# Kernel optimization log

Hardware: AMD Instinct MI355X
Metric: run time of the kernel (lower is better)

Reference implementation:

```python
import jax, jax.numpy as jnp
import numpy as np

NUM_NODES = 100_000
NUM_EDGES = 1_200_000
NUM_REL = 3
EMBED_DIM = 64
HIDDEN_DIM = 64
NUM_CLS = 2
NUM_GRAPHS = 512


def setup_inputs() -> dict:
    key = jax.random.key(0)
    ks = jax.random.split(key, 12)
    s = 1.0 / np.sqrt(EMBED_DIM)
    inp = {
        # forward args
        "x": jnp.zeros((NUM_NODES,), dtype=jnp.int64),  # vocab size 1 -> all zeros
        "edge_index": jax.random.randint(ks[0], (2, NUM_EDGES), 0, NUM_NODES, dtype=jnp.int64),
        "edge_type": jax.random.randint(ks[1], (NUM_EDGES,), 0, NUM_REL, dtype=jnp.int64),
        "batch": jnp.sort(jax.random.randint(ks[2], (NUM_NODES,), 0, NUM_GRAPHS, dtype=jnp.int64)),
        # parameters
        "embed_w": jax.random.normal(ks[3], (1, EMBED_DIM), jnp.float32),
        "W1": jax.random.normal(ks[4], (NUM_REL, EMBED_DIM, HIDDEN_DIM), jnp.float32) * s,
        "root1": jax.random.normal(ks[5], (EMBED_DIM, HIDDEN_DIM), jnp.float32) * s,
        "b1": jnp.zeros((HIDDEN_DIM,), jnp.float32),
        "W2": jax.random.normal(ks[6], (NUM_REL, HIDDEN_DIM, HIDDEN_DIM), jnp.float32) * s,
        "root2": jax.random.normal(ks[7], (HIDDEN_DIM, HIDDEN_DIM), jnp.float32) * s,
        "b2": jnp.zeros((HIDDEN_DIM,), jnp.float32),
        "lin_w": jax.random.normal(ks[8], (HIDDEN_DIM, NUM_CLS), jnp.float32) * s,
        "lin_b": jnp.zeros((NUM_CLS,), jnp.float32),
    }
    return inp


def rgcn_conv(h, W, root, b, src, dst, edge_type):
    """PyG RGCNConv with mean aggregation per relation + root weight + bias."""
    n = h.shape[0]
    out = h @ root + b  # root/self contribution, [N, H]
    for r in range(NUM_REL):
        m = (edge_type == r).astype(h.dtype)  # [E]
        tr = h @ W[r]                          # [N, H] small GEMM
        msg = tr[src] * m[:, None]             # gather [E, H]
        ssum = jax.ops.segment_sum(msg, dst, num_segments=n)  # scatter-add [N, H]
        cnt = jax.ops.segment_sum(m, dst, num_segments=n)     # per-relation in-degree
        out = out + ssum / jnp.clip(cnt, 1.0)[:, None]        # mean aggregation
    return out


def reference(x, edge_index, edge_type, batch, embed_w, W1, root1, b1, W2, root2, b2, lin_w, lin_b):
    src, dst = edge_index[0], edge_index[1]
    h = embed_w[x]                                       # [N, D] embedding lookup
    h = jax.nn.relu(rgcn_conv(h, W1, root1, b1, src, dst, edge_type))
    h = jax.nn.relu(rgcn_conv(h, W2, root2, b2, src, dst, edge_type))
    # global mean pool over graphs
    gsum = jax.ops.segment_sum(h, batch, num_segments=NUM_GRAPHS)            # [G, H]
    gcnt = jax.ops.segment_sum(jnp.ones_like(h[:, 0]), batch, num_segments=NUM_GRAPHS)
    g_emb = gsum / jnp.clip(gcnt, 1.0)[:, None]
    return g_emb @ lin_w + lin_b                          # [G, num_cls]
```

## Files before the change

kernel.cpp:

```cpp
#include <hip/hip_runtime.h>

#define NODES   100000
#define EDGES   1200000
#define NREL    3
#define DIM     64
#define NGRAPH  512

#define NB      98
#define BSH     10
#define BUCKCAP 16384
#define SBLK    256
#define CHUNK   4688
#define PBS     128

#define OFF_GSUM  0
#define OFF_GCNT  131072
#define OFF_CUR   133120
#define OFF_ZEND  133632
#define OFF_CNT   133632
#define OFF_MASK  2533632
#define OFF_REC   2633728
#define OFF_H1    9056256
#define OFF_BASE  9058304
#define OFF_T2    9060352

__global__ void k_tab1(const float* __restrict__ embed_w, const float* __restrict__ W1,
                       const float* __restrict__ root1, const float* __restrict__ b1,
                       float* __restrict__ H1) {
    __shared__ float h0[DIM];
    __shared__ float u[DIM];
    __shared__ float t[NREL][DIM];
    const int tid = threadIdx.x;
    const int j = tid & 63, w = tid >> 6;
    if (tid < DIM) h0[tid] = embed_w[tid];
    __syncthreads();
    const float* M = (w == 0) ? root1 : (W1 + (size_t)(w - 1) * DIM * DIM);
    float s = 0.f;
    for (int k = 0; k < DIM; ++k) s += h0[k] * M[k * DIM + j];
    if (w == 0) u[j] = s + b1[j];
    else        t[w - 1][j] = s;
    __syncthreads();
    for (int p = w; p < 8; p += 4) {
        float v = u[j];
        if (p & 1) v += t[0][j];
        if (p & 2) v += t[1][j];
        if (p & 4) v += t[2][j];
        H1[p * DIM + j] = fmaxf(v, 0.f);
    }
}

__global__ void k_tab2(const float* __restrict__ H1, const float* __restrict__ root2,
                       const float* __restrict__ b2, const float* __restrict__ W2,
                       float* __restrict__ base, float* __restrict__ T2) {
    __shared__ float hrow[DIM];
    __shared__ float red[4][DIM];
    const int tid = threadIdx.x;
    const int j = tid & 63, kq = tid >> 6;
    const int row = blockIdx.x;
    const int p = (row < 8) ? row : ((row - 8) & 7);
    if (tid < DIM) hrow[tid] = H1[p * DIM + tid];
    __syncthreads();
    const float* M = (row < 8) ? root2 : (W2 + (size_t)((row - 8) >> 3) * DIM * DIM);
    float s = 0.f;
    for (int k = kq * 16; k < kq * 16 + 16; ++k) s += hrow[k] * M[k * DIM + j];
    red[kq][j] = s;
    __syncthreads();
    if (kq == 0) {
        const float v = red[0][j] + red[1][j] + red[2][j] + red[3][j];
        if (row < 8) base[p * DIM + j] = v + b2[j];
        else         T2[(row - 8) * DIM + j] = v;
    }
}

__global__ void k_scatter(const int* __restrict__ ei, const int* __restrict__ et,
                          int* __restrict__ cursor, unsigned int* __restrict__ rec) {
    __shared__ int hist[PBS];
    __shared__ int cur[PBS];
    const int tid = threadIdx.x;
    if (tid < PBS) hist[tid] = 0;
    __syncthreads();
    const int e0 = blockIdx.x * CHUNK;
    const int* src = ei;
    const int* dst = ei + EDGES;
    for (int i = tid; i < CHUNK / 4; i += 256) {
        const int e = e0 + i * 4;
        if (e < EDGES) {
            const int4 d4 = *(const int4*)(dst + e);
            atomicAdd(&hist[d4.x >> BSH], 1);
            atomicAdd(&hist[d4.y >> BSH], 1);
            atomicAdd(&hist[d4.z >> BSH], 1);
            atomicAdd(&hist[d4.w >> BSH], 1);
        }
    }
    __syncthreads();
    if (tid < PBS) {
        const int h = hist[tid];
        const int r = h ? atomicAdd(&cursor[tid], h) : 0;
        cur[tid] = tid * BUCKCAP + r;
    }
    __syncthreads();
    const int lim = (NB) * BUCKCAP;  (void)lim;
    for (int i = tid; i < CHUNK / 4; i += 256) {
        const int e = e0 + i * 4;
        if (e < EDGES) {
            const int4 s4 = *(const int4*)(src + e);
            const int4 d4 = *(const int4*)(dst + e);
            const int4 r4 = *(const int4*)(et + e);
            int p;
            p = atomicAdd(&cur[d4.x >> BSH], 1);
            if (p < ((d4.x >> BSH) + 1) * BUCKCAP)
                rec[p] = ((unsigned)(d4.x & 1023) << 19) | ((unsigned)r4.x << 17) | (unsigned)s4.x;
            p = atomicAdd(&cur[d4.y >> BSH], 1);
            if (p < ((d4.y >> BSH) + 1) * BUCKCAP)
                rec[p] = ((unsigned)(d4.y & 1023) << 19) | ((unsigned)r4.y << 17) | (unsigned)s4.y;
            p = atomicAdd(&cur[d4.z >> BSH], 1);
            if (p < ((d4.z >> BSH) + 1) * BUCKCAP)
                rec[p] = ((unsigned)(d4.z & 1023) << 19) | ((unsigned)r4.z << 17) | (unsigned)s4.z;
            p = atomicAdd(&cur[d4.w >> BSH], 1);
            if (p < ((d4.w >> BSH) + 1) * BUCKCAP)
                rec[p] = ((unsigned)(d4.w & 1023) << 19) | ((unsigned)r4.w << 17) | (unsigned)s4.w;
        }
    }
}

__global__ void k_deg(const unsigned int* __restrict__ rec, const int* __restrict__ cursor,
                      unsigned char* __restrict__ mask) {
    __shared__ int deg[1024 * NREL];
    const int tid = threadIdx.x;
    for (int i = tid; i < 1024 * NREL; i += 1024) deg[i] = 0;
    __syncthreads();
    const int b = blockIdx.x;
    const int s = b * BUCKCAP;
    const int n = cursor[b];
    for (int i = tid; i < n; i += 1024) {
        const unsigned r32 = rec[s + i];
        atomicAdd(&deg[(r32 >> 19) * NREL + ((r32 >> 17) & 3)], 1);
    }
    __syncthreads();
    const int v = (b << BSH) + tid;
    if (v < NODES) {
        const int d0 = deg[tid * 3], d1 = deg[tid * 3 + 1], d2 = deg[tid * 3 + 2];
        mask[v] = (unsigned char)((d0 ? 1 : 0) | (d1 ? 2 : 0) | (d2 ? 4 : 0));
    }
}

__global__ void k_hist(const unsigned int* __restrict__ rec, const int* __restrict__ cursor,
                       const unsigned char* __restrict__ mask,
                       unsigned long long* __restrict__ cnt) {
    __shared__ unsigned int h[1024 * 24 / 2];
    const int tid = threadIdx.x;
    for (int i = tid; i < 12288; i += 1024) h[i] = 0;
    __syncthreads();
    const int b = blockIdx.x;
    const int s = b * BUCKCAP;
    const int n = cursor[b];
    for (int i = tid; i < n; i += 1024) {
        const unsigned r32 = rec[s + i];
        const int idx = (r32 >> 19) * 24 + ((r32 >> 17) & 3) * 8 + mask[r32 & 0x1FFFF];
        atomicAdd(&h[idx >> 1], 1u << ((idx & 1) * 16));
    }
    __syncthreads();
    const int v = (b << BSH) + tid;
    if (v < NODES) {
        const int w0 = tid * 12;
        for (int r = 0; r < NREL; ++r) {
            unsigned long long w = 0;
            #pragma unroll
            for (int q = 0; q < 4; ++q) {
                const unsigned x = h[w0 + r * 4 + q];
                w |= ((unsigned long long)(x & 0xFFFFu) << (16 * q))
                   | ((unsigned long long)(x >> 16)    << (16 * q + 8));
            }
            cnt[(size_t)v * 3 + r] = w;
        }
    }
}

__global__ void k_node(const unsigned char* __restrict__ mask,
                       const unsigned long long* __restrict__ cnt,
                       const int* __restrict__ batch,
                       const float* __restrict__ base, const float* __restrict__ T2,
                       float* __restrict__ gsum, int* __restrict__ gcnt) {
    __shared__ float bs[8 * DIM];
    __shared__ float ts[24 * DIM];
    const int tid = threadIdx.x;
    for (int i = tid; i < 8 * DIM; i += 256) bs[i] = base[i];
    for (int i = tid; i < 24 * DIM; i += 256) ts[i] = T2[i];
    __syncthreads();
    const int lane = tid & 63;
    const int grp = blockIdx.x * 4 + (tid >> 6);
    const int v0 = grp * 8;
    if (v0 >= NODES) return;
    float acc = 0.f;
    int curg = -1, runlen = 0;
    for (int i = 0; i < 8; ++i) {
        const int v = v0 + i;
        if (v >= NODES) break;
        float s = bs[mask[v] * DIM + lane];
        for (int r = 0; r < NREL; ++r) {
            const unsigned long long w = cnt[(size_t)v * 3 + r];
            float msg = 0.f;
            int cr = 0;
            #pragma unroll
            for (int p = 0; p < 8; ++p) {
                const int c = (int)((w >> (8 * p)) & 0xFF);
                cr += c;
                msg += (float)c * ts[(r * 8 + p) * DIM + lane];
            }
            s += msg / fmaxf((float)cr, 1.0f);
        }
        s = fmaxf(s, 0.f);
        const int g = batch[v];
        if (g != curg) {
            if (curg >= 0) {
                atomicAdd(&gsum[curg * DIM + lane], acc);
                if (lane == 0) atomicAdd(&gcnt[curg], runlen);
            }
            curg = g; acc = 0.f; runlen = 0;
        }
        acc += s; runlen++;
    }
    if (curg >= 0) {
        atomicAdd(&gsum[curg * DIM + lane], acc);
        if (lane == 0) atomicAdd(&gcnt[curg], runlen);
    }
}

__global__ void k_final(const float* __restrict__ gsum, const int* __restrict__ gcnt,
                        const float* __restrict__ lin_w, const float* __restrict__ lin_b,
                        float* __restrict__ out) {
    const int lane = threadIdx.x & 63;
    const int g = blockIdx.x * (blockDim.x >> 6) + (threadIdx.x >> 6);
    if (g >= NGRAPH) return;
    const float inv = 1.0f / fmaxf((float)gcnt[g], 1.0f);
    const float s = gsum[g * DIM + lane] * inv;
    float p0 = s * lin_w[lane * 2 + 0];
    float p1 = s * lin_w[lane * 2 + 1];
    for (int off = 32; off; off >>= 1) {
        p0 += __shfl_down(p0, off);
        p1 += __shfl_down(p1, off);
    }
    if (lane == 0) {
        out[g * 2 + 0] = p0 + lin_b[0];
        out[g * 2 + 1] = p1 + lin_b[1];
    }
}

extern "C" void kernel_launch(void* const* d_in, const int* in_sizes, int n_in,
                              void* d_out, int out_size, void* d_ws, size_t ws_size,
                              hipStream_t stream) {
    const int*   ei      = (const int*)d_in[1];
    const int*   et      = (const int*)d_in[2];
    const int*   batch   = (const int*)d_in[3];
    const float* embed_w = (const float*)d_in[4];
    const float* W1      = (const float*)d_in[5];
    const float* root1   = (const float*)d_in[6];
    const float* b1      = (const float*)d_in[7];
    const float* W2      = (const float*)d_in[8];
    const float* root2   = (const float*)d_in[9];
    const float* b2      = (const float*)d_in[10];
    const float* lin_w   = (const float*)d_in[11];
    const float* lin_b   = (const float*)d_in[12];
    float* out = (float*)d_out;

    char* ws = (char*)d_ws;
    float*              gsum = (float*)(ws + OFF_GSUM);
    int*                gcnt = (int*)(ws + OFF_GCNT);
    int*                cur  = (int*)(ws + OFF_CUR);
    unsigned long long* cnt  = (unsigned long long*)(ws + OFF_CNT);
    unsigned char*      mask = (unsigned char*)(ws + OFF_MASK);
    unsigned int*       rec  = (unsigned int*)(ws + OFF_REC);
    float*              H1   = (float*)(ws + OFF_H1);
    float*              base = (float*)(ws + OFF_BASE);
    float*              T2   = (float*)(ws + OFF_T2);

    hipMemsetAsync(d_ws, 0, OFF_ZEND, stream);

    k_tab1   <<<1,    256, 0, stream>>>(embed_w, W1, root1, b1, H1);
    k_tab2   <<<32,   256, 0, stream>>>(H1, root2, b2, W2, base, T2);
    k_scatter<<<SBLK, 256, 0, stream>>>(ei, et, cur, rec);
    k_deg    <<<NB,  1024, 0, stream>>>(rec, cur, mask);
    k_hist   <<<NB,  1024, 0, stream>>>(rec, cur, mask, cnt);
    k_node   <<<3125, 256, 0, stream>>>(mask, cnt, batch, base, T2, gsum, gcnt);
    k_final  <<<128,  256, 0, stream>>>(gsum, gcnt, lin_w, lin_b, out);
}
```

Measured before the change: 154.5 us.

## Use per-relation presence bytemap, smaller buckets, and fold workspace zeroing into tab kernel

Replaces the k_deg pass, which re-read all bucketed edge records to build the per-node relation mask, with byte flags written directly during the scatter and then combined by a tiny k_asm kernel. Buckets shrink from 1024 to 256 nodes, giving 391 blocks of 256 threads for the histogram pass and more parallelism. The hipMemsetAsync is removed and the workspace zeroing moves into k_tab2. The cost is extra scattered byte stores in k_scatter and a larger zeroed region. Smaller bucket capacity also raises the chance of overflow, and records past capacity would be dropped.

Result: no change. 157.4 us (+1.8%).

```diff
diff --git a/kernel.cpp b/kernel.cpp
--- a/kernel.cpp
+++ b/kernel.cpp
@@ -6,23 +6,24 @@
 #define DIM     64
 #define NGRAPH  512
 
-#define NB      98
-#define BSH     10
-#define BUCKCAP 16384
+#define BSH     8
+#define NB      391
+#define BUCKCAP 4096
 #define SBLK    256
 #define CHUNK   4688
-#define PBS     128
+#define MBPITCH 100352
 
 #define OFF_GSUM  0
 #define OFF_GCNT  131072
 #define OFF_CUR   133120
-#define OFF_ZEND  133632
-#define OFF_CNT   133632
-#define OFF_MASK  2533632
-#define OFF_REC   2633728
-#define OFF_H1    9056256
-#define OFF_BASE  9058304
-#define OFF_T2    9060352
+#define OFF_MB    135168
+#define OFF_ZEND  436224
+#define OFF_CNT   436224
+#define OFF_MASK  2836224
+#define OFF_REC   2936576
+#define OFF_H1    9342720
+#define OFF_BASE  9344768
+#define OFF_T2    9346816
 
 __global__ void k_tab1(const float* __restrict__ embed_w, const float* __restrict__ W1,
                        const float* __restrict__ root1, const float* __restrict__ b1,
@@ -51,7 +52,14 @@
 
 __global__ void k_tab2(const float* __restrict__ H1, const float* __restrict__ root2,
                        const float* __restrict__ b2, const float* __restrict__ W2,
-                       float* __restrict__ base, float* __restrict__ T2) {
+                       float* __restrict__ base, float* __restrict__ T2,
+                       char* __restrict__ ws) {
+    {
+        uint4* z = (uint4*)ws;
+        const uint4 zz = make_uint4(0, 0, 0, 0);
+        const int gt = blockIdx.x * 256 + threadIdx.x;
+        for (int i = gt; i < OFF_ZEND / 16; i += 8192) z[i] = zz;
+    }
     __shared__ float hrow[DIM];
     __shared__ float red[4][DIM];
     const int tid = threadIdx.x;
@@ -73,11 +81,12 @@
 }
 
 __global__ void k_scatter(const int* __restrict__ ei, const int* __restrict__ et,
-                          int* __restrict__ cursor, unsigned int* __restrict__ rec) {
-    __shared__ int hist[PBS];
-    __shared__ int cur[PBS];
-    const int tid = threadIdx.x;
-    if (tid < PBS) hist[tid] = 0;
+                          int* __restrict__ cursor, unsigned int* __restrict__ rec,
+                          unsigned char* __restrict__ mb) {
+    __shared__ int hist[NB];
+    __shared__ int cur[NB];
+    const int tid = threadIdx.x;
+    for (int b = tid; b < NB; b += 256) hist[b] = 0;
     __syncthreads();
     const int e0 = blockIdx.x * CHUNK;
     const int* src = ei;
@@ -93,13 +102,12 @@
         }
     }
     __syncthreads();
-    if (tid < PBS) {
-        const int h = hist[tid];
-        const int r = h ? atomicAdd(&cursor[tid], h) : 0;
-        cur[tid] = tid * BUCKCAP + r;
-    }
-    __syncthreads();
-    const int lim = (NB) * BUCKCAP;  (void)lim;
+    for (int b = tid; b < NB; b += 256) {
+        const int h = hist[b];
+        const int r = h ? atomicAdd(&cursor[b], h) : 0;
+        cur[b] = b * BUCKCAP + r;
+    }
+    __syncthreads();
     for (int i = tid; i < CHUNK / 4; i += 256) {
         const int e = e0 + i * 4;
         if (e < EDGES) {
@@ -109,52 +117,51 @@
             int p;
             p = atomicAdd(&cur[d4.x >> BSH], 1);
             if (p < ((d4.x >> BSH) + 1) * BUCKCAP)
-                rec[p] = ((unsigned)(d4.x & 1023) << 19) | ((unsigned)r4.x << 17) | (unsigned)s4.x;
+                rec[p] = ((unsigned)(d4.x & 255) << 19) | ((unsigned)r4.x << 17) | (unsigned)s4.x;
+            mb[r4.x * MBPITCH + d4.x] = 1;
             p = atomicAdd(&cur[d4.y >> BSH], 1);
             if (p < ((d4.y >> BSH) + 1) * BUCKCAP)
-                rec[p] = ((unsigned)(d4.y & 1023) << 19) | ((unsigned)r4.y << 17) | (unsigned)s4.y;
+                rec[p] = ((unsigned)(d4.y & 255) << 19) | ((unsigned)r4.y << 17) | (unsigned)s4.y;
+            mb[r4.y * MBPITCH + d4.y] = 1;
             p = atomicAdd(&cur[d4.z >> BSH], 1);
             if (p < ((d4.z >> BSH) + 1) * BUCKCAP)
-                rec[p] = ((unsigned)(d4.z & 1023) << 19) | ((unsigned)r4.z << 17) | (unsigned)s4.z;
+                rec[p] = ((unsigned)(d4.z & 255) << 19) | ((unsigned)r4.z << 17) | (unsigned)s4.z;
+            mb[r4.z * MBPITCH + d4.z] = 1;
             p = atomicAdd(&cur[d4.w >> BSH], 1);
             if (p < ((d4.w >> BSH) + 1) * BUCKCAP)
-                rec[p] = ((unsigned)(d4.w & 1023) << 19) | ((unsigned)r4.w << 17) | (unsigned)s4.w;
-        }
-    }
-}
-
-__global__ void k_deg(const unsigned int* __restrict__ rec, const int* __restrict__ cursor,
+                rec[p] = ((unsigned)(d4.w & 255) << 19) | ((unsigned)r4.w << 17) | (unsigned)s4.w;
+            mb[r4.w * MBPITCH + d4.w] = 1;
+        }
+    }
+}
+
+__global__ void k_asm(const unsigned char* __restrict__ mb,
                       unsigned char* __restrict__ mask) {
-    __shared__ int deg[1024 * NREL];
-    const int tid = threadIdx.x;
-    for (int i = tid; i < 1024 * NREL; i += 1024) deg[i] = 0;
-    __syncthreads();
-    const int b = blockIdx.x;
-    const int s = b * BUCKCAP;
-    const int n = cursor[b];
-    for (int i = tid; i < n; i += 1024) {
-        const unsigned r32 = rec[s + i];
-        atomicAdd(&deg[(r32 >> 19) * NREL + ((r32 >> 17) & 3)], 1);
-    }
-    __syncthreads();
-    const int v = (b << BSH) + tid;
-    if (v < NODES) {
-        const int d0 = deg[tid * 3], d1 = deg[tid * 3 + 1], d2 = deg[tid * 3 + 2];
-        mask[v] = (unsigned char)((d0 ? 1 : 0) | (d1 ? 2 : 0) | (d2 ? 4 : 0));
-    }
+    const int v = (blockIdx.x * blockDim.x + threadIdx.x) * 4;
+    if (v >= NODES) return;
+    const uchar4 a = *(const uchar4*)(mb + v);
+    const uchar4 b = *(const uchar4*)(mb + MBPITCH + v);
+    const uchar4 c = *(const uchar4*)(mb + 2 * MBPITCH + v);
+    uchar4 o;
+    o.x = (unsigned char)(a.x | (b.x << 1) | (c.x << 2));
+    o.y = (unsigned char)(a.y | (b.y << 1) | (c.y << 2));
+    o.z = (unsigned char)(a.z | (b.z << 1) | (c.z << 2));
+    o.w = (unsigned char)(a.w | (b.w << 1) | (c.w << 2));
+    *(uchar4*)(mask + v) = o;
 }
 
 __global__ void k_hist(const unsigned int* __restrict__ rec, const int* __restrict__ cursor,
                        const unsigned char* __restrict__ mask,
                        unsigned long long* __restrict__ cnt) {
-    __shared__ unsigned int h[1024 * 24 / 2];
-    const int tid = threadIdx.x;
-    for (int i = tid; i < 12288; i += 1024) h[i] = 0;
+    __shared__ unsigned int h[256 * 24 / 2];
+    const int tid = threadIdx.x;
+    for (int i = tid; i < 3072; i += 256) h[i] = 0;
     __syncthreads();
     const int b = blockIdx.x;
     const int s = b * BUCKCAP;
-    const int n = cursor[b];
-    for (int i = tid; i < n; i += 1024) {
+    int n = cursor[b];
+    if (n > BUCKCAP) n = BUCKCAP;
+    for (int i = tid; i < n; i += 256) {
         const unsigned r32 = rec[s + i];
         const int idx = (r32 >> 19) * 24 + ((r32 >> 17) & 3) * 8 + mask[r32 & 0x1FFFF];
         atomicAdd(&h[idx >> 1], 1u << ((idx & 1) * 16));
@@ -267,6 +274,7 @@
     float*              gsum = (float*)(ws + OFF_GSUM);
     int*                gcnt = (int*)(ws + OFF_GCNT);
     int*                cur  = (int*)(ws + OFF_CUR);
+    unsigned char*      mb   = (unsigned char*)(ws + OFF_MB);
     unsigned long long* cnt  = (unsigned long long*)(ws + OFF_CNT);
     unsigned char*      mask = (unsigned char*)(ws + OFF_MASK);
     unsigned int*       rec  = (unsigned int*)(ws + OFF_REC);
@@ -274,13 +282,11 @@
     float*              base = (float*)(ws + OFF_BASE);
     float*              T2   = (float*)(ws + OFF_T2);
 
-    hipMemsetAsync(d_ws, 0, OFF_ZEND, stream);
-
     k_tab1   <<<1,    256, 0, stream>>>(embed_w, W1, root1, b1, H1);
-    k_tab2   <<<32,   256, 0, stream>>>(H1, root2, b2, W2, base, T2);
-    k_scatter<<<SBLK, 256, 0, stream>>>(ei, et, cur, rec);
-    k_deg    <<<NB,  1024, 0, stream>>>(rec, cur, mask);
-    k_hist   <<<NB,  1024, 0, stream>>>(rec, cur, mask, cnt);
+    k_tab2   <<<32,   256, 0, stream>>>(H1, root2, b2, W2, base, T2, ws);
+    k_scatter<<<SBLK, 256, 0, stream>>>(ei, et, cur, rec, mb);
+    k_asm    <<<98,   256, 0, stream>>>(mb, mask);
+    k_hist   <<<NB,   256, 0, stream>>>(rec, cur, mask, cnt);
     k_node   <<<3125, 256, 0, stream>>>(mask, cnt, batch, base, T2, gsum, gcnt);
     k_final  <<<128,  256, 0, stream>>>(gsum, gcnt, lin_w, lin_b, out);
 }
```
